# Performance work log

Measured on AMD Instinct MI355X. Metric: run time of the kernel, lower is better.

## Reference

```python
import jax, jax.numpy as jnp
import numpy as np

NUM_LABELS = 50
LABEL_COUNT = 8
D = 512


def setup_inputs() -> dict:
    key = jax.random.key(0)
    k1, k2, k3, k4, k5, k6 = jax.random.split(key, 6)
    B, S = 16, 4096
    return {
        "text_hidden": jax.random.normal(k1, (B, S, D), dtype=jnp.float32),
        "text_mask": jnp.ones((B, S), dtype=bool),
        "des_hidden": jax.random.normal(k2, (NUM_LABELS * LABEL_COUNT, D), dtype=jnp.float32),
        "Ww": jax.random.normal(k3, (D, D), dtype=jnp.float32) * (1.0 / np.sqrt(D)),
        "bw": jax.random.normal(k4, (D,), dtype=jnp.float32) * 0.01,
        "Wb": jax.random.normal(k5, (D, 1), dtype=jnp.float32) * (1.0 / np.sqrt(D)),
        "bb": jax.random.normal(k6, (1,), dtype=jnp.float32) * 0.01,
    }


def reference(text_hidden, text_mask, des_hidden, Ww, bw, Wb, bb):
    # text_hidden: [B, S, D]; des_hidden: [50*8, D]; text_mask unused (as in source).
    label = des_hidden.reshape(NUM_LABELS, LABEL_COUNT, D)  # [L, C, D]
    # score: 'abd,ecd->aebc' -> [B, L, S, C]
    score = jnp.einsum('bsd,lcd->blsc', text_hidden, label)
    alpha = jax.nn.softmax(score, axis=2)  # softmax over seq dim
    # m = einsum('abd,aebc->aedc') then sum over c  ==  einsum('bsd,blsc->bld')
    m = jnp.einsum('bsd,blsc->bld', text_hidden, alpha)  # [B, L, D]
    des = label.max(axis=1)  # [L, D]
    w = jax.nn.leaky_relu(des @ Ww + bw)        # [L, D]
    b = jax.nn.leaky_relu(des @ Wb + bb)        # [L, 1]
    logits = jnp.einsum('bld,ld->bl', m, w) + b[:, 0]  # [B, L]
    return logits
```

## Files before the change

kernel.cpp:

```cpp
#include <hip/hip_runtime.h>
#include <math.h>

#define B_ 16
#define S_ 4096
#define D_ 512
#define L_ 50
#define C_ 8
#define N_ 400

typedef __attribute__((ext_vector_type(8))) short bf16x8;
typedef __attribute__((ext_vector_type(4))) float f32x4;

__device__ __forceinline__ void split_bf16(float x, unsigned short& h, unsigned short& l) {
    unsigned int xb = __float_as_uint(x);
    unsigned int hb = (xb + 0x8000u) & 0xffff0000u;
    float lf = x - __uint_as_float(hb);
    h = (unsigned short)(hb >> 16);
    l = (unsigned short)((__float_as_uint(lf) + 0x8000u) >> 16);
}

#define BM1 128
#define BN1 80
#define KC1 32
#define LDK 40

__global__ __launch_bounds__(256) void k1_score_mfma(const float* __restrict__ text,
                                                     const float* __restrict__ des,
                                                     float* __restrict__ score_t) {
    __shared__ unsigned short th[BM1][LDK];
    __shared__ unsigned short tl[BM1][LDK];
    __shared__ unsigned short dh[BN1][LDK];
    __shared__ unsigned short dl[BN1][LDK];

    const int nwg = gridDim.x * gridDim.y;
    int wg = blockIdx.y * gridDim.x + blockIdx.x;
    int q = nwg >> 3;
    int sw = (wg & 7) * q + (wg >> 3);
    const int ntile = sw % 5;
    const int mtile = sw / 5;

    const int tid = threadIdx.x;
    const int r0 = mtile * BM1;
    const int n0 = ntile * BN1;
    const int b  = r0 >> 12;
    const int s0 = r0 & (S_ - 1);

    const int wave = tid >> 6;
    const int lane = tid & 63;
    const int lrow = lane & 15;
    const int lkg  = lane >> 4;

    f32x4 acc[5][2];
    #pragma unroll
    for (int i = 0; i < 5; ++i)
        #pragma unroll
        for (int j = 0; j < 2; ++j) acc[i][j] = (f32x4){0.f, 0.f, 0.f, 0.f};

    for (int kc = 0; kc < D_; kc += KC1) {
        #pragma unroll
        for (int i = 0; i < 4; ++i) {
            int idx = tid + i * 256;
            int row = idx >> 3;
            int kq  = (idx & 7) * 4;
            float4 v = *(const float4*)&text[(size_t)(r0 + row) * D_ + kc + kq];
            unsigned short h0,h1,h2,h3,l0,l1,l2,l3;
            split_bf16(v.x,h0,l0); split_bf16(v.y,h1,l1);
            split_bf16(v.z,h2,l2); split_bf16(v.w,h3,l3);
            *(ushort4*)&th[row][kq] = make_ushort4(h0,h1,h2,h3);
            *(ushort4*)&tl[row][kq] = make_ushort4(l0,l1,l2,l3);
        }
        for (int p = tid; p < 640; p += 256) {
            int row = p >> 3;
            int kq  = (p & 7) * 4;
            float4 v = *(const float4*)&des[(size_t)(n0 + row) * D_ + kc + kq];
            unsigned short h0,h1,h2,h3,l0,l1,l2,l3;
            split_bf16(v.x,h0,l0); split_bf16(v.y,h1,l1);
            split_bf16(v.z,h2,l2); split_bf16(v.w,h3,l3);
            *(ushort4*)&dh[row][kq] = make_ushort4(h0,h1,h2,h3);
            *(ushort4*)&dl[row][kq] = make_ushort4(l0,l1,l2,l3);
        }
        __syncthreads();

        bf16x8 fdh[5], fdl[5], fth[2], ftl[2];
        #pragma unroll
        for (int nf = 0; nf < 5; ++nf) {
            int row = nf * 16 + lrow;
            fdh[nf] = *(const bf16x8*)&dh[row][lkg * 8];
            fdl[nf] = *(const bf16x8*)&dl[row][lkg * 8];
        }
        #pragma unroll
        for (int mf = 0; mf < 2; ++mf) {
            int row = wave * 32 + mf * 16 + lrow;
            fth[mf] = *(const bf16x8*)&th[row][lkg * 8];
            ftl[mf] = *(const bf16x8*)&tl[row][lkg * 8];
        }
        #pragma unroll
        for (int nf = 0; nf < 5; ++nf)
            #pragma unroll
            for (int mf = 0; mf < 2; ++mf) {
                acc[nf][mf] = __builtin_amdgcn_mfma_f32_16x16x32_bf16(fdh[nf], fth[mf], acc[nf][mf], 0, 0, 0);
                acc[nf][mf] = __builtin_amdgcn_mfma_f32_16x16x32_bf16(fdh[nf], ftl[mf], acc[nf][mf], 0, 0, 0);
                acc[nf][mf] = __builtin_amdgcn_mfma_f32_16x16x32_bf16(fdl[nf], fth[mf], acc[nf][mf], 0, 0, 0);
            }
        __syncthreads();
    }

    #pragma unroll
    for (int nf = 0; nf < 5; ++nf) {
        #pragma unroll
        for (int mf = 0; mf < 2; ++mf) {
            int s = s0 + wave * 32 + mf * 16 + (lane & 15);
            #pragma unroll
            for (int r = 0; r < 4; ++r) {
                int n = n0 + nf * 16 + (lane >> 4) * 4 + r;
                score_t[((size_t)b * N_ + n) * S_ + s] = acc[nf][mf][r];
            }
        }
    }
}

__global__ __launch_bounds__(512) void k2_softmax_A(const float* __restrict__ score_t,
                                                    float* __restrict__ A) {
    const int l = blockIdx.x;
    const int b = blockIdx.y;
    const int tid = threadIdx.x;
    const int c = tid >> 6;
    const int lane = tid & 63;
    __shared__ float cm[8], ci[8];

    const float4* row = (const float4*)(score_t + ((size_t)b * N_ + l * 8 + c) * S_);
    float v[64];
    #pragma unroll
    for (int i = 0; i < 16; ++i) {
        float4 x = row[lane + 64 * i];
        v[4*i] = x.x; v[4*i+1] = x.y; v[4*i+2] = x.z; v[4*i+3] = x.w;
    }
    float lm = v[0];
    #pragma unroll
    for (int i = 1; i < 64; ++i) lm = fmaxf(lm, v[i]);
    #pragma unroll
    for (int off = 32; off > 0; off >>= 1) lm = fmaxf(lm, __shfl_xor(lm, off, 64));
    float ls = 0.f;
    #pragma unroll
    for (int i = 0; i < 64; ++i) ls += __expf(v[i] - lm);
    #pragma unroll
    for (int off = 32; off > 0; off >>= 1) ls += __shfl_xor(ls, off, 64);
    if (lane == 0) { cm[c] = lm; ci[c] = 1.f / ls; }
    __syncthreads();

    float4* Arow = (float4*)(A + ((size_t)b * L_ + l) * S_);
    #pragma unroll
    for (int h = 0; h < 2; ++h) {
        int p = tid + h * 512;
        float4 a = make_float4(0.f, 0.f, 0.f, 0.f);
        #pragma unroll
        for (int cc = 0; cc < 8; ++cc) {
            const float4* r2 = (const float4*)(score_t + ((size_t)b * N_ + l * 8 + cc) * S_);
            float4 x = r2[p];
            float mm = cm[cc], iv = ci[cc];
            a.x += __expf(x.x - mm) * iv;
            a.y += __expf(x.y - mm) * iv;
            a.z += __expf(x.z - mm) * iv;
            a.w += __expf(x.w - mm) * iv;
        }
        Arow[p] = a;
    }
}

#define DT3 128
#define ST3 64
#define KSPLIT 8

__global__ __launch_bounds__(256) void k3_mgemm(const float* __restrict__ text,
                                                const float* __restrict__ A,
                                                float* __restrict__ mp) {
    const int dt = blockIdx.x;
    const int b  = blockIdx.y;
    const int ks = blockIdx.z;
    const int tid = threadIdx.x;
    const int tx = tid & 31;
    const int ty = tid >> 5;
    __shared__ float Ts[ST3][DT3 + 4];
    __shared__ float Asb[L_][ST3 + 4];

    const int d0 = dt * DT3;
    const int s_begin = ks * (S_ / KSPLIT);

    float acc[7][4];
    #pragma unroll
    for (int i = 0; i < 7; ++i)
        #pragma unroll
        for (int j = 0; j < 4; ++j) acc[i][j] = 0.f;

    for (int sc = 0; sc < S_ / KSPLIT; sc += ST3) {
        const int s0 = s_begin + sc;
        #pragma unroll
        for (int i = 0; i < 8; ++i) {
            int p = tid + i * 256;
            int row = p >> 5;
            int col = (p & 31) * 4;
            float4 v = *(const float4*)&text[((size_t)b * S_ + s0 + row) * D_ + d0 + col];
            *(float4*)&Ts[row][col] = v;
        }
        for (int p = tid; p < 800; p += 256) {
            int row = p >> 4;
            int col = (p & 15) * 4;
            float4 v = *(const float4*)&A[((size_t)b * L_ + row) * S_ + s0 + col];
            *(float4*)&Asb[row][col] = v;
        }
        __syncthreads();
        for (int sl = 0; sl < ST3; ++sl) {
            float4 t4 = *(const float4*)&Ts[sl][tx * 4];
            #pragma unroll
            for (int i = 0; i < 6; ++i) {
                float a = Asb[ty + 8 * i][sl];
                acc[i][0] += a * t4.x;
                acc[i][1] += a * t4.y;
                acc[i][2] += a * t4.z;
                acc[i][3] += a * t4.w;
            }
            if (ty < 2) {
                float a = Asb[ty + 48][sl];
                acc[6][0] += a * t4.x;
                acc[6][1] += a * t4.y;
                acc[6][2] += a * t4.z;
                acc[6][3] += a * t4.w;
            }
        }
        __syncthreads();
    }

    #pragma unroll
    for (int i = 0; i < 7; ++i) {
        int l = ty + 8 * i;
        if (l < L_) {
            float* dst = &mp[(((size_t)ks * B_ + b) * L_ + l) * D_ + d0 + tx * 4];
            *(float4*)dst = make_float4(acc[i][0], acc[i][1], acc[i][2], acc[i][3]);
        }
    }
}

__global__ __launch_bounds__(512) void k4a(const float* __restrict__ des,
                                           const float* __restrict__ Ww,
                                           const float* __restrict__ bw,
                                           const float* __restrict__ Wb,
                                           const float* __restrict__ bbv,
                                           float* __restrict__ w_buf,
                                           float* __restrict__ bvec) {
    const int l = blockIdx.x;
    const int tid = threadIdx.x;
    __shared__ float des_l[D_];
    __shared__ float red[512];

    float mx = -INFINITY;
    #pragma unroll
    for (int c = 0; c < 8; ++c)
        mx = fmaxf(mx, des[(size_t)(l * 8 + c) * D_ + tid]);
    des_l[tid] = mx;
    __syncthreads();

    float s = bw[tid];
    #pragma unroll 4
    for (int k = 0; k < D_; ++k)
        s += des_l[k] * Ww[(size_t)k * D_ + tid];
    w_buf[(size_t)l * D_ + tid] = s > 0.f ? s : 0.01f * s;

    red[tid] = des_l[tid] * Wb[tid];
    __syncthreads();
    for (int off = 256; off > 0; off >>= 1) {
        if (tid < off) red[tid] += red[tid + off];
        __syncthreads();
    }
    if (tid == 0) {
        float v = red[0] + bbv[0];
        bvec[l] = v > 0.f ? v : 0.01f * v;
    }
}

__global__ __launch_bounds__(64) void k4b(const float* __restrict__ mp,
                                          const float* __restrict__ w_buf,
                                          const float* __restrict__ bvec,
                                          float* __restrict__ out) {
    const int l = blockIdx.x;
    const int b = blockIdx.y;
    const int lane = threadIdx.x;
    float acc = 0.f;
    #pragma unroll
    for (int i = 0; i < 8; ++i) {
        int d = lane + 64 * i;
        float msum = 0.f;
        #pragma unroll
        for (int ks = 0; ks < KSPLIT; ++ks)
            msum += mp[(((size_t)ks * B_ + b) * L_ + l) * D_ + d];
        acc += msum * w_buf[(size_t)l * D_ + d];
    }
    #pragma unroll
    for (int off = 32; off > 0; off >>= 1) acc += __shfl_xor(acc, off, 64);
    if (lane == 0) out[b * L_ + l] = acc + bvec[l];
}

extern "C" void kernel_launch(void* const* d_in, const int* in_sizes, int n_in,
                              void* d_out, int out_size, void* d_ws, size_t ws_size,
                              hipStream_t stream) {
    const float* text = (const float*)d_in[0];
    const float* des  = (const float*)d_in[2];
    const float* Ww   = (const float*)d_in[3];
    const float* bw   = (const float*)d_in[4];
    const float* Wb   = (const float*)d_in[5];
    const float* bbv  = (const float*)d_in[6];
    float* out = (float*)d_out;

    float* score_t = (float*)d_ws;
    float* A       = score_t + (size_t)B_ * N_ * S_;
    float* w_buf   = A + (size_t)B_ * L_ * S_;
    float* bvec    = w_buf + (size_t)L_ * D_;
    float* mp      = score_t;

    k1_score_mfma<<<dim3(5, (B_ * S_) / BM1), 256, 0, stream>>>(text, des, score_t);
    k2_softmax_A<<<dim3(L_, B_), 512, 0, stream>>>(score_t, A);
    k3_mgemm<<<dim3(D_ / DT3, B_, KSPLIT), 256, 0, stream>>>(text, A, mp);
    k4a<<<L_, 512, 0, stream>>>(des, Ww, bw, Wb, bbv, w_buf, bvec);
    k4b<<<dim3(L_, B_), 64, 0, stream>>>(mp, w_buf, bvec, out);
}
```

Baseline: 540.5 us.

## Pre-split text and label embeddings into bf16 hi/lo buffers before score GEMM

Adds preprocessing kernels that convert the fp32 text and label matrices into separate bf16 high/low arrays in workspace once. The score GEMM then loads ready-made bf16 halves and prefetches the next K chunk into registers while computing the current one. The aim is to stop every tile (text reloaded by 5 N-tiles) from redoing the split, and to overlap global loads with MFMA work. In exchange it adds an extra full pass over the 128MB text tensor plus 64MB of writes, and falls back to the old kernel if the workspace is too small.

```diff
diff --git a/kernel.cpp b/kernel.cpp
--- a/kernel.cpp
+++ b/kernel.cpp
@@ -10,6 +10,7 @@
 
 typedef __attribute__((ext_vector_type(8))) short bf16x8;
 typedef __attribute__((ext_vector_type(4))) float f32x4;
+typedef unsigned short u16;
 
 __device__ __forceinline__ void split_bf16(float x, unsigned short& h, unsigned short& l) {
     unsigned int xb = __float_as_uint(x);
@@ -19,18 +20,169 @@
     l = (unsigned short)((__float_as_uint(lf) + 0x8000u) >> 16);
 }
 
+__global__ __launch_bounds__(256) void k0_text(const float* __restrict__ x,
+                                               u16* __restrict__ hi, u16* __restrict__ lo) {
+    const size_t n4 = (size_t)B_ * S_ * D_ / 4;
+    for (size_t i = (size_t)blockIdx.x * 256 + threadIdx.x; i < n4; i += (size_t)gridDim.x * 256) {
+        float4 v = ((const float4*)x)[i];
+        unsigned short h0,h1,h2,h3,l0,l1,l2,l3;
+        split_bf16(v.x,h0,l0); split_bf16(v.y,h1,l1);
+        split_bf16(v.z,h2,l2); split_bf16(v.w,h3,l3);
+        ((ushort4*)hi)[i] = make_ushort4(h0,h1,h2,h3);
+        ((ushort4*)lo)[i] = make_ushort4(l0,l1,l2,l3);
+    }
+}
+
+__global__ __launch_bounds__(256) void k0_des(const float* __restrict__ x,
+                                              u16* __restrict__ hi, u16* __restrict__ lo) {
+    const int i = blockIdx.x * 256 + threadIdx.x;
+    if (i < N_ * D_ / 4) {
+        float4 v = ((const float4*)x)[i];
+        unsigned short h0,h1,h2,h3,l0,l1,l2,l3;
+        split_bf16(v.x,h0,l0); split_bf16(v.y,h1,l1);
+        split_bf16(v.z,h2,l2); split_bf16(v.w,h3,l3);
+        ((ushort4*)hi)[i] = make_ushort4(h0,h1,h2,h3);
+        ((ushort4*)lo)[i] = make_ushort4(l0,l1,l2,l3);
+    }
+}
+
 #define BM1 128
 #define BN1 80
 #define KC1 32
 #define LDK 40
-
-__global__ __launch_bounds__(256) void k1_score_mfma(const float* __restrict__ text,
+#define NCHUNK 16
+
+__global__ __launch_bounds__(256) void k1_score_v2(const u16* __restrict__ th_g,
+                                                   const u16* __restrict__ tl_g,
+                                                   const u16* __restrict__ dh_g,
+                                                   const u16* __restrict__ dl_g,
+                                                   float* __restrict__ score_t) {
+    __shared__ u16 th[BM1][LDK];
+    __shared__ u16 tl[BM1][LDK];
+    __shared__ u16 dh[BN1][LDK];
+    __shared__ u16 dl[BN1][LDK];
+
+    const int nwg = gridDim.x * gridDim.y;
+    int wg = blockIdx.y * gridDim.x + blockIdx.x;
+    int q = nwg >> 3;
+    int sw = (wg & 7) * q + (wg >> 3);
+    const int ntile = sw % 5;
+    const int mtile = sw / 5;
+
+    const int tid = threadIdx.x;
+    const int r0 = mtile * BM1;
+    const int n0 = ntile * BN1;
+    const int b  = r0 >> 12;
+    const int s0 = r0 & (S_ - 1);
+
+    const int wave = tid >> 6;
+    const int lane = tid & 63;
+    const int lrow = lane & 15;
+    const int lkg  = lane >> 4;
+
+    f32x4 acc[5][2];
+    #pragma unroll
+    for (int i = 0; i < 5; ++i)
+        #pragma unroll
+        for (int j = 0; j < 2; ++j) acc[i][j] = (f32x4){0.f, 0.f, 0.f, 0.f};
+
+    ushort4 rth[4], rtl[4], rdh[3], rdl[3];
+
+    auto load_chunk = [&](int kc) {
+        #pragma unroll
+        for (int i = 0; i < 4; ++i) {
+            int idx = tid + i * 256;
+            int row = idx >> 3;
+            int kq  = (idx & 7) * 4;
+            size_t g = (size_t)(r0 + row) * D_ + kc + kq;
+            rth[i] = *(const ushort4*)&th_g[g];
+            rtl[i] = *(const ushort4*)&tl_g[g];
+        }
+        #pragma unroll
+        for (int i = 0; i < 3; ++i) {
+            int p = tid + i * 256;
+            if (p < 640) {
+                int row = p >> 3;
+                int kq  = (p & 7) * 4;
+                size_t g = (size_t)(n0 + row) * D_ + kc + kq;
+                rdh[i] = *(const ushort4*)&dh_g[g];
+                rdl[i] = *(const ushort4*)&dl_g[g];
+            }
+        }
+    };
+    auto write_chunk = [&]() {
+        #pragma unroll
+        for (int i = 0; i < 4; ++i) {
+            int idx = tid + i * 256;
+            int row = idx >> 3;
+            int kq  = (idx & 7) * 4;
+            *(ushort4*)&th[row][kq] = rth[i];
+            *(ushort4*)&tl[row][kq] = rtl[i];
+        }
+        #pragma unroll
+        for (int i = 0; i < 3; ++i) {
+            int p = tid + i * 256;
+            if (p < 640) {
+                int row = p >> 3;
+                int kq  = (p & 7) * 4;
+                *(ushort4*)&dh[row][kq] = rdh[i];
+                *(ushort4*)&dl[row][kq] = rdl[i];
+            }
+        }
+    };
+
+    load_chunk(0);
+
+    for (int ck = 0; ck < NCHUNK; ++ck) {
+        __syncthreads();
+        write_chunk();
+        __syncthreads();
+        if (ck + 1 < NCHUNK) load_chunk((ck + 1) * KC1);
+
+        bf16x8 fdh[5], fdl[5], fth[2], ftl[2];
+        #pragma unroll
+        for (int nf = 0; nf < 5; ++nf) {
+            int row = nf * 16 + lrow;
+            fdh[nf] = *(const bf16x8*)&dh[row][lkg * 8];
+            fdl[nf] = *(const bf16x8*)&dl[row][lkg * 8];
+        }
+        #pragma unroll
+        for (int mf = 0; mf < 2; ++mf) {
+            int row = wave * 32 + mf * 16 + lrow;
+            fth[mf] = *(const bf16x8*)&th[row][lkg * 8];
+            ftl[mf] = *(const bf16x8*)&tl[row][lkg * 8];
+        }
+        #pragma unroll
+        for (int nf = 0; nf < 5; ++nf)
+            #pragma unroll
+            for (int mf = 0; mf < 2; ++mf) {
+                acc[nf][mf] = __builtin_amdgcn_mfma_f32_16x16x32_bf16(fdh[nf], fth[mf], acc[nf][mf], 0, 0, 0);
+                acc[nf][mf] = __builtin_amdgcn_mfma_f32_16x16x32_bf16(fdh[nf], ftl[mf], acc[nf][mf], 0, 0, 0);
+                acc[nf][mf] = __builtin_amdgcn_mfma_f32_16x16x32_bf16(fdl[nf], fth[mf], acc[nf][mf], 0, 0, 0);
+            }
+    }
+
+    #pragma unroll
+    for (int nf = 0; nf < 5; ++nf) {
+        #pragma unroll
+        for (int mf = 0; mf < 2; ++mf) {
+            int s = s0 + wave * 32 + mf * 16 + (lane & 15);
+            #pragma unroll
+            for (int r = 0; r < 4; ++r) {
+                int n = n0 + nf * 16 + (lane >> 4) * 4 + r;
+                score_t[((size_t)b * N_ + n) * S_ + s] = acc[nf][mf][r];
+            }
+        }
+    }
+}
+
+__global__ __launch_bounds__(256) void k1_score_conv(const float* __restrict__ text,
                                                      const float* __restrict__ des,
                                                      float* __restrict__ score_t) {
-    __shared__ unsigned short th[BM1][LDK];
-    __shared__ unsigned short tl[BM1][LDK];
-    __shared__ unsigned short dh[BN1][LDK];
-    __shared__ unsigned short dl[BN1][LDK];
+    __shared__ u16 th[BM1][LDK];
+    __shared__ u16 tl[BM1][LDK];
+    __shared__ u16 dh[BN1][LDK];
+    __shared__ u16 dl[BN1][LDK];
 
     const int nwg = gridDim.x * gridDim.y;
     int wg = blockIdx.y * gridDim.x + blockIdx.x;
@@ -310,13 +462,26 @@
     const float* bbv  = (const float*)d_in[6];
     float* out = (float*)d_out;
 
-    float* score_t = (float*)d_ws;
+    float* ws = (float*)d_ws;
+    float* score_t = ws;
     float* A       = score_t + (size_t)B_ * N_ * S_;
     float* w_buf   = A + (size_t)B_ * L_ * S_;
     float* bvec    = w_buf + (size_t)L_ * D_;
     float* mp      = score_t;
 
-    k1_score_mfma<<<dim3(5, (B_ * S_) / BM1), 256, 0, stream>>>(text, des, score_t);
+    u16* th_g = (u16*)(bvec + 64);
+    u16* tl_g = th_g + (size_t)B_ * S_ * D_;
+    u16* dh_g = tl_g + (size_t)B_ * S_ * D_;
+    u16* dl_g = dh_g + (size_t)N_ * D_;
+    size_t needed = (size_t)((char*)(dl_g + (size_t)N_ * D_) - (char*)d_ws);
+
+    if (ws_size >= needed) {
+        k0_text<<<2048, 256, 0, stream>>>(text, th_g, tl_g);
+        k0_des<<<200, 256, 0, stream>>>(des, dh_g, dl_g);
+        k1_score_v2<<<dim3(5, (B_ * S_) / BM1), 256, 0, stream>>>(th_g, tl_g, dh_g, dl_g, score_t);
+    } else {
+        k1_score_conv<<<dim3(5, (B_ * S_) / BM1), 256, 0, stream>>>(text, des, score_t);
+    }
     k2_softmax_A<<<dim3(L_, B_), 512, 0, stream>>>(score_t, A);
     k3_mgemm<<<dim3(D_ / DT3, B_, KSPLIT), 256, 0, stream>>>(text, A, mp);
     k4a<<<L_, 512, 0, stream>>>(des, Ww, bw, Wb, bbv, w_buf, bvec);
```

After: 518.4 us. -4.1%, faster.
